# Kernel optimization log

Hardware: AMD Instinct MI355X
Metric: run time of the kernel (lower is better)

Reference implementation:

```python
import jax, jax.numpy as jnp
import numpy as np

B, S, D, H = 2, 2048, 1024, 16
HD = D // H  # head_dim = 64


def setup_inputs() -> dict:
    key = jax.random.key(0)
    ks = jax.random.split(key, 12)
    s = 0.02
    return {
        "x": jax.random.normal(ks[0], (B, S, D), jnp.float32),
        "mask": jnp.ones((B, 1, S, S), jnp.int32),
        "Wq": jax.random.normal(ks[1], (D, D), jnp.float32) * s,
        "bq": jnp.zeros((D,), jnp.float32),
        "Wk": jax.random.normal(ks[2], (D, D), jnp.float32) * s,
        "bk": jnp.zeros((D,), jnp.float32),
        "Wv": jax.random.normal(ks[3], (D, D), jnp.float32) * s,
        "bv": jnp.zeros((D,), jnp.float32),
        "Wo": jax.random.normal(ks[4], (D, D), jnp.float32) * s,
        "bo": jnp.zeros((D,), jnp.float32),
        "W1": jax.random.normal(ks[5], (D, 4 * D), jnp.float32) * s,
        "b1": jnp.zeros((4 * D,), jnp.float32),
        "W2": jax.random.normal(ks[6], (4 * D, D), jnp.float32) * s,
        "b2": jnp.zeros((D,), jnp.float32),
        "gamma": jnp.ones((D,), jnp.float32),
        "beta": jnp.zeros((D,), jnp.float32),
    }


def reference(x, mask, Wq, bq, Wk, bk, Wv, bv, Wo, bo, W1, b1, W2, b2, gamma, beta):
    b, s, d = x.shape
    # QKV projections -> [b, h, s, hd]
    q = (x @ Wq + bq).reshape(b, s, H, HD).transpose(0, 2, 1, 3)
    k = (x @ Wk + bk).reshape(b, s, H, HD).transpose(0, 2, 1, 3)
    v = (x @ Wv + bv).reshape(b, s, H, HD).transpose(0, 2, 1, 3)
    # manual attention: full [b, h, s, s] score matrix (as in the torch code)
    scores = jnp.einsum("bhqd,bhkd->bhqk", q, k) / jnp.sqrt(jnp.float32(HD))
    causal = jnp.tril(mask)  # mask.tril(), broadcasts over heads
    scores = jnp.where(causal == 0, jnp.float32(-1e9), scores)
    attn = jax.nn.softmax(scores, axis=-1)  # dropout is identity in eval
    out = jnp.einsum("bhqk,bhkd->bhqd", attn, v)
    out = out.transpose(0, 2, 1, 3).reshape(b, s, d)
    attn_out = out @ Wo + bo  # NOTE: no residual / no layernorm after attention (faithful)
    # FFN with exact GELU, residual, post-LayerNorm (eps=1e-6)
    h = jax.nn.gelu(attn_out @ W1 + b1, approximate=False)
    down = h @ W2 + b2
    y = attn_out + down
    mu = jnp.mean(y, axis=-1, keepdims=True)
    var = jnp.var(y, axis=-1, keepdims=True)
    return (y - mu) / jnp.sqrt(var + 1e-6) * gamma + beta
```

## Files before the change

### kernel.cpp

```cpp
#include <hip/hip_runtime.h>
#include <hip/hip_bf16.h>
#include <cmath>
#include <cstdint>

typedef __hip_bfloat16 bf16;
typedef __attribute__((ext_vector_type(4))) float f32x4;
typedef __attribute__((ext_vector_type(16))) float f32x16;
typedef __attribute__((ext_vector_type(8))) short s16x8;
typedef __attribute__((ext_vector_type(4))) unsigned int u32x4;
typedef __attribute__((ext_vector_type(2))) unsigned int u32x2;

#define NB 2
#define NS 2048
#define ND 1024
#define NH 16
#define NHD 64

static __device__ __forceinline__ bf16 f2bf(float v){ return __float2bfloat16(v); }
static __device__ __forceinline__ unsigned short f2bfu(float v){
  bf16 b = __float2bfloat16(v);
  return *reinterpret_cast<unsigned short*>(&b);
}
static __device__ __forceinline__ float bfu2f(unsigned short u){
  union { unsigned int i; float f; } c; c.i = ((unsigned int)u) << 16; return c.f;
}

static __device__ __forceinline__ void gload_lds16(const void* g, void* l){
  __builtin_amdgcn_global_load_lds((const __attribute__((address_space(1))) void*)g,
                                   (__attribute__((address_space(3))) void*)l, 16, 0, 0);
}


__global__ __launch_bounds__(256) void convert_kernel(const float* __restrict__ src,
                                                       unsigned short* __restrict__ dst, int n4){
  int i = blockIdx.x * 256 + threadIdx.x;
  if (i >= n4) return;
  float4 v = ((const float4*)src)[i];
  ushort4 o;
  o.x = f2bfu(v.x); o.y = f2bfu(v.y); o.z = f2bfu(v.z); o.w = f2bfu(v.w);
  ((ushort4*)dst)[i] = o;
}

__global__ __launch_bounds__(256) void transpose_convert(const float* __restrict__ src,
                                                          bf16* __restrict__ dst, int R, int C){
  __shared__ float tile[32][33];
  int c0 = blockIdx.x * 32, r0 = blockIdx.y * 32;
  int tx = threadIdx.x & 31, ty = threadIdx.x >> 5;
  #pragma unroll
  for (int i = ty; i < 32; i += 8)
    tile[i][tx] = src[(size_t)(r0 + i) * C + c0 + tx];
  __syncthreads();
  #pragma unroll
  for (int i = ty; i < 32; i += 8)
    dst[(size_t)(c0 + i) * R + r0 + tx] = f2bf(tile[tx][i]);
}

__global__ void pack_bias_kernel(const float* __restrict__ bq, const float* __restrict__ bk,
                                 const float* __restrict__ bv, float* __restrict__ dst){
  int i = blockIdx.x * 256 + threadIdx.x;
  if (i < 1024) dst[i] = bq[i];
  else if (i < 2048) dst[i] = bk[i - 1024];
  else if (i < 3072) dst[i] = bv[i - 2048];
}

template<int EPI, int BM>
__global__ __launch_bounds__(256)
void gemm_bf16(const bf16* __restrict__ A, const bf16* __restrict__ BT,
               const float* __restrict__ bias, bf16* __restrict__ C,
               bf16* __restrict__ kP, bf16* __restrict__ vB, int M, int N, int K)
{
  constexpr int MF = BM / 32;
  constexpr int RA = BM / 64;
  __shared__ bf16 As[2][BM * 32];
  __shared__ bf16 Bs[2][128 * 32];

  const int tid = threadIdx.x;
  const int lane = tid & 63;
  const int wave = tid >> 6;
  const int lr = lane & 15, lg = lane >> 4;
  const int wm = wave >> 1, wn = wave & 1;

  const int nbx = N >> 7;
  const int nwg = gridDim.x;
  const int wg = blockIdx.x;
  const int swz = (wg & 7) * (nwg >> 3) + (wg >> 3);
  const int bx = swz % nbx, by = swz / nbx;
  const int m0 = by * BM, n0 = bx << 7;

  f32x4 acc[MF][4] = {};

  const int NT = K >> 5;

  auto stage = [&](int t, int buf){
    const int k0 = t << 5;
    #pragma unroll
    for (int rch = 0; rch < RA; ++rch){
      int e = (rch * 256 + tid) * 8;
      int row = e >> 5, col = e & 31;
      gload_lds16(A + (size_t)(m0 + row) * K + k0 + col, &As[buf][e]);
    }
    #pragma unroll
    for (int rch = 0; rch < 2; ++rch){
      int e = (rch * 256 + tid) * 8;
      int row = e >> 5, col = e & 31;
      gload_lds16(BT + (size_t)(n0 + row) * K + k0 + col, &Bs[buf][e]);
    }
  };

  stage(0, 0);
  __syncthreads();

  for (int t = 0; t < NT; ++t){
    const int cur = t & 1;
    if (t + 1 < NT) stage(t + 1, cur ^ 1);
    s16x8 af[MF], bfr[4];
    #pragma unroll
    for (int m = 0; m < MF; ++m)
      af[m] = *(const s16x8*)&As[cur][(wm * (BM / 2) + m * 16 + lr) * 32 + lg * 8];
    #pragma unroll
    for (int n = 0; n < 4; ++n)
      bfr[n] = *(const s16x8*)&Bs[cur][(wn * 64 + n * 16 + lr) * 32 + lg * 8];
    #pragma unroll
    for (int m = 0; m < MF; ++m)
      #pragma unroll
      for (int n = 0; n < 4; ++n)
        acc[m][n] = __builtin_amdgcn_mfma_f32_16x16x32_bf16(af[m], bfr[n], acc[m][n], 0, 0, 0);
    __syncthreads();
  }

  if (EPI == 1 && n0 >= 2048){
    #pragma unroll
    for (int n = 0; n < 4; ++n){
      const int col = n0 + wn * 64 + n * 16 + lr;
      const float bv = bias[col];
      const int c2 = col - 2048, h = c2 >> 6, d = c2 & 63;
      #pragma unroll
      for (int m = 0; m < MF; ++m){
        const int row = m0 + wm * (BM / 2) + m * 16 + lg * 4;
        const int b = row >> 11, sq = row & 2047;
        unsigned int lo = (unsigned int)f2bfu(acc[m][n][0] + bv) | ((unsigned int)f2bfu(acc[m][n][1] + bv) << 16);
        unsigned int hi2 = (unsigned int)f2bfu(acc[m][n][2] + bv) | ((unsigned int)f2bfu(acc[m][n][3] + bv) << 16);
        u32x2 val; val[0] = lo; val[1] = hi2;
        const size_t idx = (((size_t)(b * NH + h) * 64 + (sq >> 5)) * 64 + d) * 32 + (sq & 31);
        *(u32x2*)&vB[idx] = val;
      }
    }
  } else if (EPI == 1 && n0 >= 1024){
    #pragma unroll
    for (int n = 0; n < 4; ++n){
      const int col = n0 + wn * 64 + n * 16 + lr;
      const float bv = bias[col];
      const int c2 = col - 1024, h = c2 >> 6, d = c2 & 63;
      #pragma unroll
      for (int m = 0; m < MF; ++m){
        #pragma unroll
        for (int r = 0; r < 4; ++r){
          const int row = m0 + wm * (BM / 2) + m * 16 + lg * 4 + r;
          const int b = row >> 11, sq = row & 2047;
          kP[((size_t)(b * NH + h) * 2048 + sq) * 64 + d] = f2bf(acc[m][n][r] + bv);
        }
      }
    }
  } else {
    #pragma unroll
    for (int n = 0; n < 4; ++n){
      const int col = n0 + wn * 64 + n * 16 + lr;
      const float bv = bias[col];
      #pragma unroll
      for (int m = 0; m < MF; ++m){
        #pragma unroll
        for (int r = 0; r < 4; ++r){
          const int row = m0 + wm * (BM / 2) + m * 16 + lg * 4 + r;
          float v = acc[m][n][r] + bv;
          if (EPI == 2) v = 0.5f * v * (1.f + erff(v * 0.70710678118f));
          C[(size_t)row * N + col] = f2bf(v);
        }
      }
    }
  }
}

template<int EPI>
__global__ __launch_bounds__(512, 2)
void gemm256(const bf16* __restrict__ A, const bf16* __restrict__ BT,
             const float* __restrict__ bias, bf16* __restrict__ C,
             char* __restrict__ wsbase, int M, int N, int K)
{
  __shared__ bf16 As[2][256 * 64];
  __shared__ bf16 Bs[2][256 * 64];

  const int tid = threadIdx.x;
  const int lane = tid & 63, wave = tid >> 6;
  const int lr = lane & 15, lg = lane >> 4;
  const int wm = wave >> 2, wn = wave & 3;

  const int nwg = gridDim.x;
  const int wg = blockIdx.x;
  const int s = (wg & 7) * (nwg >> 3) + (wg >> 3);

  int m0, n0, kbase, NT;
  bf16* outp;
  int ldo;
  if (EPI == 3){
    const int kc = s >> 6, tile = s & 63;
    m0 = (tile >> 2) << 8; n0 = (tile & 3) << 8;
    kbase = kc << 10; NT = 16;
    size_t off = (kc < 2) ? (size_t)kc * 8388608u
                          : 33566720u + (size_t)(kc - 2) * 8388608u;
    outp = (bf16*)(wsbase + off); ldo = 1024;
  } else {
    const int nbx = N >> 8;
    m0 = (s / nbx) << 8; n0 = (s % nbx) << 8;
    kbase = 0; NT = K >> 6;
    outp = C; ldo = N;
  }

  auto stage = [&](int t, int buf){
    const int k0 = kbase + (t << 6);
    #pragma unroll
    for (int j = 0; j < 4; ++j){
      const int bi = j * 512 + tid;
      const int row = bi >> 3, slot = bi & 7;
      const int ss = slot ^ (row & 7);
      gload_lds16(A + (size_t)(m0 + row) * K + k0 + ss * 8,
                  (char*)(&As[buf][0]) + bi * 16);
    }
    #pragma unroll
    for (int j = 0; j < 4; ++j){
      const int bi = j * 512 + tid;
      const int row = bi >> 3, slot = bi & 7;
      const int ss = slot ^ (row & 7);
      gload_lds16(BT + (size_t)(n0 + row) * K + k0 + ss * 8,
                  (char*)(&Bs[buf][0]) + bi * 16);
    }
  };

  f32x4 acc[8][4] = {};
  const int rsx = lr & 7;

  stage(0, 0);
  __syncthreads();

  #pragma unroll 1
  for (int G = 0; G < NT; ++G){
    const int X = G & 1;
    if (G + 1 < NT) stage(G + 1, X ^ 1);

    s16x8 bfr[4][2];
    #pragma unroll
    for (int n = 0; n < 4; ++n){
      const int rowb = wn * 64 + n * 16 + lr;
      #pragma unroll
      for (int kk = 0; kk < 2; ++kk){
        const int slot = ((kk << 2) + lg) ^ rsx;
        bfr[n][kk] = *(const s16x8*)((const char*)(&Bs[X][0]) + rowb * 128 + slot * 16);
      }
    }
    #pragma unroll
    for (int p = 0; p < 4; ++p){
      s16x8 af[2][2];
      #pragma unroll
      for (int m2 = 0; m2 < 2; ++m2){
        const int rowa = wm * 128 + (p * 2 + m2) * 16 + lr;
        #pragma unroll
        for (int kk = 0; kk < 2; ++kk){
          const int slot = ((kk << 2) + lg) ^ rsx;
          af[m2][kk] = *(const s16x8*)((const char*)(&As[X][0]) + rowa * 128 + slot * 16);
        }
      }
      #pragma unroll
      for (int m2 = 0; m2 < 2; ++m2)
        #pragma unroll
        for (int n = 0; n < 4; ++n){
          acc[p * 2 + m2][n] = __builtin_amdgcn_mfma_f32_16x16x32_bf16(af[m2][0], bfr[n][0], acc[p * 2 + m2][n], 0, 0, 0);
          acc[p * 2 + m2][n] = __builtin_amdgcn_mfma_f32_16x16x32_bf16(af[m2][1], bfr[n][1], acc[p * 2 + m2][n], 0, 0, 0);
        }
    }
    __syncthreads();
  }

  #pragma unroll
  for (int n = 0; n < 4; ++n){
    const int col = n0 + wn * 64 + n * 16 + lr;
    const float bv = (EPI == 3) ? 0.f : bias[col];
    #pragma unroll
    for (int m = 0; m < 8; ++m){
      #pragma unroll
      for (int r = 0; r < 4; ++r){
        const int row = m0 + wm * 128 + m * 16 + lg * 4 + r;
        float v = acc[m][n][r] + bv;
        if (EPI == 2) v = 0.5f * v * (1.f + erff(v * 0.70710678118f));
        outp[(size_t)row * ldo + col] = f2bf(v);
      }
    }
  }
}

__global__ __launch_bounds__(256, 3)
void attn_kernel(const bf16* __restrict__ qkv, const bf16* __restrict__ kP,
                 const bf16* __restrict__ vB, bf16* __restrict__ out)
{
  const int j = blockIdx.x;
  const int bh = j & 31, p = j >> 5;
  const int b = bh >> 4, h = bh & 15;
  const int tid = threadIdx.x, lane = tid & 63, wave = tid >> 6;
  const int l31 = lane & 31, hi = lane >> 5;
  const int strip = (wave < 2) ? (63 - p) : p;
  const int hsel = wave & 1, sidx = wave >> 1;
  const int q0 = strip * 32;

  __shared__ float Ob[2][32 * 64];
  __shared__ float Lb[2][32];

  auto scale8 = [](s16x8 v){
    s16x8 o;
    #pragma unroll
    for (int i = 0; i < 8; ++i){
      unsigned short u = (unsigned short)v[i];
      unsigned short e = u & 0x7F80;
      o[i] = (short)(e > (3 << 7) ? (unsigned short)(u - (3 << 7)) : (unsigned short)(u & 0x8000));
    }
    return o;
  };

  const bf16* qbase = qkv + (size_t)(b * NS + q0 + l31) * 3072 + h * 64 + hi * 8;
  s16x8 qf[4];
  #pragma unroll
  for (int kk = 0; kk < 4; ++kk)
    qf[kk] = scale8(*(const s16x8*)(qbase + kk * 16));

  const bf16* kpb = kP + (size_t)bh * 2048 * 64;
  const bf16* vbb = vB + (size_t)bh * 64 * 64 * 32;

  f32x16 oacc0 = {}, oacc1 = {};
  float lsum = 0.f;

  #pragma unroll 1
  for (int t = hsel; t <= strip; t += 2){
    const bf16* krow = kpb + (size_t)(t * 32 + l31) * 64 + hi * 8;
    s16x8 kf0 = *(const s16x8*)(krow);
    s16x8 kf1 = *(const s16x8*)(krow + 16);
    s16x8 kf2 = *(const s16x8*)(krow + 32);
    s16x8 kf3 = *(const s16x8*)(krow + 48);
    const bf16* vt0 = vbb + ((size_t)t * 64 + l31) * 32 + hi * 8;
    const bf16* vt1 = vbb + ((size_t)t * 64 + 32 + l31) * 32 + hi * 8;
    s16x8 vf00 = *(const s16x8*)(vt0);
    s16x8 vf10 = *(const s16x8*)(vt0 + 16);
    s16x8 vf01 = *(const s16x8*)(vt1);
    s16x8 vf11 = *(const s16x8*)(vt1 + 16);

    f32x16 sacc = {};
    sacc = __builtin_amdgcn_mfma_f32_32x32x16_bf16(kf0, qf[0], sacc, 0, 0, 0);
    sacc = __builtin_amdgcn_mfma_f32_32x32x16_bf16(kf1, qf[1], sacc, 0, 0, 0);
    sacc = __builtin_amdgcn_mfma_f32_32x32x16_bf16(kf2, qf[2], sacc, 0, 0, 0);
    sacc = __builtin_amdgcn_mfma_f32_32x32x16_bf16(kf3, qf[3], sacc, 0, 0, 0);

    const bool dg = (t == strip);
    float pv[16];
    #pragma unroll
    for (int r = 0; r < 16; ++r){
      const int kloc = (r & 3) + 8 * (r >> 2) + 4 * hi;
      float e = __expf(sacc[r]);
      if (dg && kloc > l31) e = 0.f;
      pv[r] = e;
      lsum += e;
    }
    unsigned int w[8];
    #pragma unroll
    for (int i = 0; i < 8; ++i)
      w[i] = (unsigned int)f2bfu(pv[2 * i]) | ((unsigned int)f2bfu(pv[2 * i + 1]) << 16);
    unsigned int s0 = hi ? w[0] : w[2];
    unsigned int s1 = hi ? w[1] : w[3];
    unsigned int s2 = hi ? w[4] : w[6];
    unsigned int s3 = hi ? w[5] : w[7];
    unsigned int g0 = (unsigned int)__shfl_xor((int)s0, 32);
    unsigned int g1 = (unsigned int)__shfl_xor((int)s1, 32);
    unsigned int g2 = (unsigned int)__shfl_xor((int)s2, 32);
    unsigned int g3 = (unsigned int)__shfl_xor((int)s3, 32);
    union { u32x4 u; s16x8 s; } pa0, pa1;
    if (hi == 0){
      pa0.u[0] = w[0]; pa0.u[1] = w[1]; pa0.u[2] = g0; pa0.u[3] = g1;
      pa1.u[0] = w[4]; pa1.u[1] = w[5]; pa1.u[2] = g2; pa1.u[3] = g3;
    } else {
      pa0.u[0] = g0; pa0.u[1] = g1; pa0.u[2] = w[2]; pa0.u[3] = w[3];
      pa1.u[0] = g2; pa1.u[1] = g3; pa1.u[2] = w[6]; pa1.u[3] = w[7];
    }
    oacc0 = __builtin_amdgcn_mfma_f32_32x32x16_bf16(pa0.s, vf00, oacc0, 0, 0, 0);
    oacc0 = __builtin_amdgcn_mfma_f32_32x32x16_bf16(pa1.s, vf10, oacc0, 0, 0, 0);
    oacc1 = __builtin_amdgcn_mfma_f32_32x32x16_bf16(pa0.s, vf01, oacc1, 0, 0, 0);
    oacc1 = __builtin_amdgcn_mfma_f32_32x32x16_bf16(pa1.s, vf11, oacc1, 0, 0, 0);
  }

  lsum += __shfl_xor(lsum, 32);
  if (hsel == 0){
    #pragma unroll
    for (int r = 0; r < 16; ++r){
      const int rowq = (r & 3) + 8 * (r >> 2) + 4 * hi;
      Ob[sidx][rowq * 64 + l31] = oacc0[r];
      Ob[sidx][rowq * 64 + 32 + l31] = oacc1[r];
    }
    if (hi == 0) Lb[sidx][l31] = lsum;
    __syncthreads();
  } else {
    __syncthreads();
    float lf = lsum + Lb[sidx][l31];
    if (hi == 0) Lb[sidx][l31] = lf;
    #pragma unroll
    for (int r = 0; r < 16; ++r){
      const int rowq = (r & 3) + 8 * (r >> 2) + 4 * hi;
      const float denom = Lb[sidx][rowq];
      const float o0 = oacc0[r] + Ob[sidx][rowq * 64 + l31];
      const float o1 = oacc1[r] + Ob[sidx][rowq * 64 + 32 + l31];
      const size_t rbase = (size_t)(b * NS + q0 + rowq) * ND + h * 64;
      out[rbase + l31] = f2bf(o0 / denom);
      out[rbase + 32 + l31] = f2bf(o1 / denom);
    }
  }
}

__global__ __launch_bounds__(256)
void ln_kernel(const bf16* __restrict__ a, const bf16* __restrict__ p0,
               const bf16* __restrict__ p1, const bf16* __restrict__ p2,
               const bf16* __restrict__ p3, const float* __restrict__ badd,
               const float* __restrict__ gamma, const float* __restrict__ beta,
               float* __restrict__ out)
{
  const int row = blockIdx.x;
  const int tid = threadIdx.x;
  const int lane = tid & 63, wave = tid >> 6;
  const size_t base = (size_t)row * ND;
  ushort4 ua = *(const ushort4*)((const unsigned short*)a  + base + tid * 4);
  ushort4 u0 = *(const ushort4*)((const unsigned short*)p0 + base + tid * 4);
  ushort4 u1 = *(const ushort4*)((const unsigned short*)p1 + base + tid * 4);
  ushort4 u2 = *(const ushort4*)((const unsigned short*)p2 + base + tid * 4);
  ushort4 u3 = *(const ushort4*)((const unsigned short*)p3 + base + tid * 4);
  float4 vb = *(const float4*)(badd + tid * 4);
  float y[4];
  y[0] = bfu2f(ua.x) + bfu2f(u0.x) + bfu2f(u1.x) + bfu2f(u2.x) + bfu2f(u3.x) + vb.x;
  y[1] = bfu2f(ua.y) + bfu2f(u0.y) + bfu2f(u1.y) + bfu2f(u2.y) + bfu2f(u3.y) + vb.y;
  y[2] = bfu2f(ua.z) + bfu2f(u0.z) + bfu2f(u1.z) + bfu2f(u2.z) + bfu2f(u3.z) + vb.z;
  y[3] = bfu2f(ua.w) + bfu2f(u0.w) + bfu2f(u1.w) + bfu2f(u2.w) + bfu2f(u3.w) + vb.w;
  float s = y[0] + y[1] + y[2] + y[3];
  float ss = y[0]*y[0] + y[1]*y[1] + y[2]*y[2] + y[3]*y[3];
  #pragma unroll
  for (int off = 1; off < 64; off <<= 1){
    s  += __shfl_xor(s, off);
    ss += __shfl_xor(ss, off);
  }
  __shared__ float rs[4], rss[4];
  if (lane == 0){ rs[wave] = s; rss[wave] = ss; }
  __syncthreads();
  const float S  = rs[0] + rs[1] + rs[2] + rs[3];
  const float SS = rss[0] + rss[1] + rss[2] + rss[3];
  const float mu = S * (1.f / 1024.f);
  const float var = SS * (1.f / 1024.f) - mu * mu;
  const float inv = rsqrtf(var + 1e-6f);
  #pragma unroll
  for (int jj = 0; jj < 4; ++jj){
    int c = tid * 4 + jj;
    out[base + c] = (y[jj] - mu) * inv * gamma[c] + beta[c];
  }
}

extern "C" void kernel_launch(void* const* d_in, const int* in_sizes, int n_in,
                              void* d_out, int out_size, void* d_ws, size_t ws_size,
                              hipStream_t stream)
{
  (void)in_sizes; (void)n_in; (void)out_size; (void)ws_size;
  const float* x  = (const float*)d_in[0];
  const float* Wq = (const float*)d_in[2];
  const float* bq = (const float*)d_in[3];
  const float* Wk = (const float*)d_in[4];
  const float* bk = (const float*)d_in[5];
  const float* Wv = (const float*)d_in[6];
  const float* bv = (const float*)d_in[7];
  const float* Wo = (const float*)d_in[8];
  const float* bo = (const float*)d_in[9];
  const float* W1 = (const float*)d_in[10];
  const float* b1 = (const float*)d_in[11];
  const float* W2 = (const float*)d_in[12];
  const float* b2 = (const float*)d_in[13];
  const float* gamma = (const float*)d_in[14];
  const float* beta  = (const float*)d_in[15];
  float* out = (float*)d_out;

  char* ws = (char*)d_ws;
  bf16* x_bf    = (bf16*)(ws + 0);
  bf16* wqkvT   = (bf16*)(ws + 8388608);
  bf16* woT     = (bf16*)(ws + 14680064);
  bf16* w1T     = (bf16*)(ws + 16777216);
  bf16* w2T     = (bf16*)(ws + 25165824);
  float* bqkv   = (float*)(ws + 33554432);
  bf16* qkv     = (bf16*)(ws + 33566720);
  bf16* vB      = (bf16*)(ws + 58732544);
  bf16* attn    = (bf16*)(ws + 67121152);
  bf16* attnout = (bf16*)(ws + 75509760);
  bf16* hbuf    = (bf16*)(ws + 92286976);
  bf16* kP      = (bf16*)(ws + 92286976);
  bf16* P0 = (bf16*)(ws + 0);
  bf16* P1 = (bf16*)(ws + 8388608);
  bf16* P2 = (bf16*)(ws + 33566720);
  bf16* P3 = (bf16*)(ws + 41955328);

  convert_kernel<<<4096, 256, 0, stream>>>(x, (unsigned short*)x_bf, 1048576);
  transpose_convert<<<dim3(32, 32), 256, 0, stream>>>(Wq, wqkvT,               1024, 1024);
  transpose_convert<<<dim3(32, 32), 256, 0, stream>>>(Wk, wqkvT + 1024 * 1024, 1024, 1024);
  transpose_convert<<<dim3(32, 32), 256, 0, stream>>>(Wv, wqkvT + 2048 * 1024, 1024, 1024);
  transpose_convert<<<dim3(32, 32), 256, 0, stream>>>(Wo, woT, 1024, 1024);
  transpose_convert<<<dim3(128, 32), 256, 0, stream>>>(W1, w1T, 1024, 4096);
  transpose_convert<<<dim3(32, 128), 256, 0, stream>>>(W2, w2T, 4096, 1024);
  pack_bias_kernel<<<12, 256, 0, stream>>>(bq, bk, bv, bqkv);

  gemm_bf16<1, 128><<<768, 256, 0, stream>>>(x_bf, wqkvT, bqkv, qkv, kP, vB, 4096, 3072, 1024);
  attn_kernel<<<dim3(1024), 256, 0, stream>>>(qkv, kP, vB, attn);
  gemm_bf16<0, 64><<<512, 256, 0, stream>>>(attn, woT, bo, attnout, nullptr, nullptr, 4096, 1024, 1024);
  gemm256<2><<<256, 512, 0, stream>>>(attnout, w1T, b1, hbuf, nullptr, 4096, 4096, 1024);
  gemm256<3><<<256, 512, 0, stream>>>(hbuf, w2T, nullptr, nullptr, ws, 4096, 1024, 4096);
  ln_kernel<<<4096, 256, 0, stream>>>(attnout, P0, P1, P2, P3, b2, gamma, beta, out);
}
```

Baseline: 250.8 us.

## Unify GEMMs into 128-wide tiled kernel with BK=64 swizzled LDS staging

Removes the 256x256 gemm256 kernel and routes the FFN up and down projections (including the split-K partial-sum path) through the 256-thread gemm_bf16 kernel with 128x128 tiles. The shared kernel now stages K=64 per step with XOR-swizzled LDS layout, halving the iteration count and reducing bank conflicts for the QKV and output projections too. Smaller tiles raise workgroup count and occupancy (launch bounds now request 2-3 blocks per CU) at the cost of lower arithmetic intensity per tile and more global traffic for the FFN GEMMs.

```diff
diff --git a/kernel.cpp b/kernel.cpp
--- a/kernel.cpp
+++ b/kernel.cpp
@@ -64,67 +64,96 @@
 }
 
 template<int EPI, int BM>
-__global__ __launch_bounds__(256)
+__global__ __launch_bounds__(256, (BM == 64) ? 3 : 2)
 void gemm_bf16(const bf16* __restrict__ A, const bf16* __restrict__ BT,
                const float* __restrict__ bias, bf16* __restrict__ C,
-               bf16* __restrict__ kP, bf16* __restrict__ vB, int M, int N, int K)
+               bf16* __restrict__ kP, bf16* __restrict__ vB,
+               char* __restrict__ wsbase, int M, int N, int K)
 {
   constexpr int MF = BM / 32;
-  constexpr int RA = BM / 64;
-  __shared__ bf16 As[2][BM * 32];
-  __shared__ bf16 Bs[2][128 * 32];
+  __shared__ bf16 As[2][BM * 64];
+  __shared__ bf16 Bs[2][128 * 64];
 
   const int tid = threadIdx.x;
-  const int lane = tid & 63;
-  const int wave = tid >> 6;
+  const int lane = tid & 63, wave = tid >> 6;
   const int lr = lane & 15, lg = lane >> 4;
   const int wm = wave >> 1, wn = wave & 1;
 
-  const int nbx = N >> 7;
-  const int nwg = gridDim.x;
-  const int wg = blockIdx.x;
-  const int swz = (wg & 7) * (nwg >> 3) + (wg >> 3);
-  const int bx = swz % nbx, by = swz / nbx;
-  const int m0 = by * BM, n0 = bx << 7;
+  const int nwg = gridDim.x, wg = blockIdx.x;
+  const int s = (wg & 7) * (nwg >> 3) + (wg >> 3);
+
+  int m0, n0, kbase, NT, ldo;
+  bf16* outp;
+  if (EPI == 3){
+    const int kc = s >> 8, tile = s & 255;
+    m0 = (tile >> 3) << 7; n0 = (tile & 7) << 7;
+    kbase = kc << 10; NT = 16;
+    size_t off = (kc < 2) ? (size_t)kc * 8388608u
+                          : 33566720u + (size_t)(kc - 2) * 8388608u;
+    outp = (bf16*)(wsbase + off); ldo = 1024;
+  } else {
+    const int nbx = N >> 7;
+    m0 = (s / nbx) * BM; n0 = (s % nbx) << 7;
+    kbase = 0; NT = K >> 6;
+    outp = C; ldo = N;
+  }
+
+  auto stage = [&](int t, int buf){
+    const int k0 = kbase + (t << 6);
+    #pragma unroll
+    for (int j = 0; j < BM / 32; ++j){
+      const int bi = j * 256 + tid;
+      const int row = bi >> 3, slot = bi & 7;
+      const int ss = slot ^ (row & 7);
+      gload_lds16(A + (size_t)(m0 + row) * K + k0 + ss * 8,
+                  (char*)(&As[buf][0]) + bi * 16);
+    }
+    #pragma unroll
+    for (int j = 0; j < 4; ++j){
+      const int bi = j * 256 + tid;
+      const int row = bi >> 3, slot = bi & 7;
+      const int ss = slot ^ (row & 7);
+      gload_lds16(BT + (size_t)(n0 + row) * K + k0 + ss * 8,
+                  (char*)(&Bs[buf][0]) + bi * 16);
+    }
+  };
 
   f32x4 acc[MF][4] = {};
-
-  const int NT = K >> 5;
-
-  auto stage = [&](int t, int buf){
-    const int k0 = t << 5;
-    #pragma unroll
-    for (int rch = 0; rch < RA; ++rch){
-      int e = (rch * 256 + tid) * 8;
-      int row = e >> 5, col = e & 31;
-      gload_lds16(A + (size_t)(m0 + row) * K + k0 + col, &As[buf][e]);
-    }
-    #pragma unroll
-    for (int rch = 0; rch < 2; ++rch){
-      int e = (rch * 256 + tid) * 8;
-      int row = e >> 5, col = e & 31;
-      gload_lds16(BT + (size_t)(n0 + row) * K + k0 + col, &Bs[buf][e]);
-    }
-  };
+  const int rsx = lr & 7;
 
   stage(0, 0);
   __syncthreads();
 
-  for (int t = 0; t < NT; ++t){
-    const int cur = t & 1;
-    if (t + 1 < NT) stage(t + 1, cur ^ 1);
-    s16x8 af[MF], bfr[4];
-    #pragma unroll
-    for (int m = 0; m < MF; ++m)
-      af[m] = *(const s16x8*)&As[cur][(wm * (BM / 2) + m * 16 + lr) * 32 + lg * 8];
-    #pragma unroll
-    for (int n = 0; n < 4; ++n)
-      bfr[n] = *(const s16x8*)&Bs[cur][(wn * 64 + n * 16 + lr) * 32 + lg * 8];
-    #pragma unroll
-    for (int m = 0; m < MF; ++m)
-      #pragma unroll
-      for (int n = 0; n < 4; ++n)
-        acc[m][n] = __builtin_amdgcn_mfma_f32_16x16x32_bf16(af[m], bfr[n], acc[m][n], 0, 0, 0);
+  #pragma unroll 1
+  for (int G = 0; G < NT; ++G){
+    const int X = G & 1;
+    if (G + 1 < NT) stage(G + 1, X ^ 1);
+
+    s16x8 bfr[4][2];
+    #pragma unroll
+    for (int n = 0; n < 4; ++n){
+      const int rowb = wn * 64 + n * 16 + lr;
+      #pragma unroll
+      for (int kk = 0; kk < 2; ++kk){
+        const int slot = ((kk << 2) + lg) ^ rsx;
+        bfr[n][kk] = *(const s16x8*)((const char*)(&Bs[X][0]) + rowb * 128 + slot * 16);
+      }
+    }
+    #pragma unroll
+    for (int m = 0; m < MF; ++m){
+      s16x8 af[2];
+      const int rowa = wm * (BM / 2) + m * 16 + lr;
+      #pragma unroll
+      for (int kk = 0; kk < 2; ++kk){
+        const int slot = ((kk << 2) + lg) ^ rsx;
+        af[kk] = *(const s16x8*)((const char*)(&As[X][0]) + rowa * 128 + slot * 16);
+      }
+      #pragma unroll
+      for (int n = 0; n < 4; ++n){
+        acc[m][n] = __builtin_amdgcn_mfma_f32_16x16x32_bf16(af[0], bfr[n][0], acc[m][n], 0, 0, 0);
+        acc[m][n] = __builtin_amdgcn_mfma_f32_16x16x32_bf16(af[1], bfr[n][1], acc[m][n], 0, 0, 0);
+      }
+    }
     __syncthreads();
   }
 
@@ -165,7 +194,7 @@
     #pragma unroll
     for (int n = 0; n < 4; ++n){
       const int col = n0 + wn * 64 + n * 16 + lr;
-      const float bv = bias[col];
+      const float bv = (EPI == 3) ? 0.f : bias[col];
       #pragma unroll
       for (int m = 0; m < MF; ++m){
         #pragma unroll
@@ -173,124 +202,8 @@
           const int row = m0 + wm * (BM / 2) + m * 16 + lg * 4 + r;
           float v = acc[m][n][r] + bv;
           if (EPI == 2) v = 0.5f * v * (1.f + erff(v * 0.70710678118f));
-          C[(size_t)row * N + col] = f2bf(v);
+          outp[(size_t)row * ldo + col] = f2bf(v);
         }
-      }
-    }
-  }
-}
-
-template<int EPI>
-__global__ __launch_bounds__(512, 2)
-void gemm256(const bf16* __restrict__ A, const bf16* __restrict__ BT,
-             const float* __restrict__ bias, bf16* __restrict__ C,
-             char* __restrict__ wsbase, int M, int N, int K)
-{
-  __shared__ bf16 As[2][256 * 64];
-  __shared__ bf16 Bs[2][256 * 64];
-
-  const int tid = threadIdx.x;
-  const int lane = tid & 63, wave = tid >> 6;
-  const int lr = lane & 15, lg = lane >> 4;
-  const int wm = wave >> 2, wn = wave & 3;
-
-  const int nwg = gridDim.x;
-  const int wg = blockIdx.x;
-  const int s = (wg & 7) * (nwg >> 3) + (wg >> 3);
-
-  int m0, n0, kbase, NT;
-  bf16* outp;
-  int ldo;
-  if (EPI == 3){
-    const int kc = s >> 6, tile = s & 63;
-    m0 = (tile >> 2) << 8; n0 = (tile & 3) << 8;
-    kbase = kc << 10; NT = 16;
-    size_t off = (kc < 2) ? (size_t)kc * 8388608u
-                          : 33566720u + (size_t)(kc - 2) * 8388608u;
-    outp = (bf16*)(wsbase + off); ldo = 1024;
-  } else {
-    const int nbx = N >> 8;
-    m0 = (s / nbx) << 8; n0 = (s % nbx) << 8;
-    kbase = 0; NT = K >> 6;
-    outp = C; ldo = N;
-  }
-
-  auto stage = [&](int t, int buf){
-    const int k0 = kbase + (t << 6);
-    #pragma unroll
-    for (int j = 0; j < 4; ++j){
-      const int bi = j * 512 + tid;
-      const int row = bi >> 3, slot = bi & 7;
-      const int ss = slot ^ (row & 7);
-      gload_lds16(A + (size_t)(m0 + row) * K + k0 + ss * 8,
-                  (char*)(&As[buf][0]) + bi * 16);
-    }
-    #pragma unroll
-    for (int j = 0; j < 4; ++j){
-      const int bi = j * 512 + tid;
-      const int row = bi >> 3, slot = bi & 7;
-      const int ss = slot ^ (row & 7);
-      gload_lds16(BT + (size_t)(n0 + row) * K + k0 + ss * 8,
-                  (char*)(&Bs[buf][0]) + bi * 16);
-    }
-  };
-
-  f32x4 acc[8][4] = {};
-  const int rsx = lr & 7;
-
-  stage(0, 0);
-  __syncthreads();
-
-  #pragma unroll 1
-  for (int G = 0; G < NT; ++G){
-    const int X = G & 1;
-    if (G + 1 < NT) stage(G + 1, X ^ 1);
-
-    s16x8 bfr[4][2];
-    #pragma unroll
-    for (int n = 0; n < 4; ++n){
-      const int rowb = wn * 64 + n * 16 + lr;
-      #pragma unroll
-      for (int kk = 0; kk < 2; ++kk){
-        const int slot = ((kk << 2) + lg) ^ rsx;
-        bfr[n][kk] = *(const s16x8*)((const char*)(&Bs[X][0]) + rowb * 128 + slot * 16);
-      }
-    }
-    #pragma unroll
-    for (int p = 0; p < 4; ++p){
-      s16x8 af[2][2];
-      #pragma unroll
-      for (int m2 = 0; m2 < 2; ++m2){
-        const int rowa = wm * 128 + (p * 2 + m2) * 16 + lr;
-        #pragma unroll
-        for (int kk = 0; kk < 2; ++kk){
-          const int slot = ((kk << 2) + lg) ^ rsx;
-          af[m2][kk] = *(const s16x8*)((const char*)(&As[X][0]) + rowa * 128 + slot * 16);
-        }
-      }
-      #pragma unroll
-      for (int m2 = 0; m2 < 2; ++m2)
-        #pragma unroll
-        for (int n = 0; n < 4; ++n){
-          acc[p * 2 + m2][n] = __builtin_amdgcn_mfma_f32_16x16x32_bf16(af[m2][0], bfr[n][0], acc[p * 2 + m2][n], 0, 0, 0);
-          acc[p * 2 + m2][n] = __builtin_amdgcn_mfma_f32_16x16x32_bf16(af[m2][1], bfr[n][1], acc[p * 2 + m2][n], 0, 0, 0);
-        }
-    }
-    __syncthreads();
-  }
-
-  #pragma unroll
-  for (int n = 0; n < 4; ++n){
-    const int col = n0 + wn * 64 + n * 16 + lr;
-    const float bv = (EPI == 3) ? 0.f : bias[col];
-    #pragma unroll
-    for (int m = 0; m < 8; ++m){
-      #pragma unroll
-      for (int r = 0; r < 4; ++r){
-        const int row = m0 + wm * 128 + m * 16 + lg * 4 + r;
-        float v = acc[m][n][r] + bv;
-        if (EPI == 2) v = 0.5f * v * (1.f + erff(v * 0.70710678118f));
-        outp[(size_t)row * ldo + col] = f2bf(v);
       }
     }
   }
@@ -511,10 +424,10 @@
   transpose_convert<<<dim3(32, 128), 256, 0, stream>>>(W2, w2T, 4096, 1024);
   pack_bias_kernel<<<12, 256, 0, stream>>>(bq, bk, bv, bqkv);
 
-  gemm_bf16<1, 128><<<768, 256, 0, stream>>>(x_bf, wqkvT, bqkv, qkv, kP, vB, 4096, 3072, 1024);
+  gemm_bf16<1, 128><<<768, 256, 0, stream>>>(x_bf, wqkvT, bqkv, qkv, kP, vB, nullptr, 4096, 3072, 1024);
   attn_kernel<<<dim3(1024), 256, 0, stream>>>(qkv, kP, vB, attn);
-  gemm_bf16<0, 64><<<512, 256, 0, stream>>>(attn, woT, bo, attnout, nullptr, nullptr, 4096, 1024, 1024);
-  gemm256<2><<<256, 512, 0, stream>>>(attnout, w1T, b1, hbuf, nullptr, 4096, 4096, 1024);
-  gemm256<3><<<256, 512, 0, stream>>>(hbuf, w2T, nullptr, nullptr, ws, 4096, 1024, 4096);
+  gemm_bf16<0, 64><<<512, 256, 0, stream>>>(attn, woT, bo, attnout, nullptr, nullptr, nullptr, 4096, 1024, 1024);
+  gemm_bf16<2, 128><<<1024, 256, 0, stream>>>(attnout, w1T, b1, hbuf, nullptr, nullptr, nullptr, 4096, 4096, 1024);
+  gemm_bf16<3, 128><<<1024, 256, 0, stream>>>(hbuf, w2T, nullptr, nullptr, nullptr, nullptr, ws, 4096, 1024, 4096);
   ln_kernel<<<4096, 256, 0, stream>>>(attnout, P0, P1, P2, P3, b2, gamma, beta, out);
 }
```

After: 243.4 us (median of 2 runs). -3.0%, faster.
